# Kernel optimization log

Measured on AMD Instinct MI355X. Metric: run time of the kernel, lower is better.

The kernel has to match this reference:

```python
import jax, jax.numpy as jnp
import numpy as np

B, L, H, E = 32, 256, 8, 16
SEQ_LEN = 64          # init seq_len, used only in final view
OUT = 256             # out_channels, must be divisible by SEQ_LEN
A = E + 1 + 128       # augmented channels: original + time + conv(128)
SIG_CH = A + A * A    # depth-2 signature channels
DN = ('NWC', 'WIO', 'NWC')


def setup_inputs() -> dict:
    key = jax.random.key(0)
    ks = jax.random.split(key, 8)
    return {
        'q': jax.random.normal(ks[0], (B, L, H, E), jnp.float32),
        'k': jax.random.normal(ks[1], (B, L, H, E), jnp.float32),
        'v': jax.random.normal(ks[2], (B, L, H, E), jnp.float32),
        'mask': jnp.zeros((B, L), jnp.bool_),
        'conv1_w': jax.random.normal(ks[3], (3, E, 64), jnp.float32) * 0.1,
        'conv1_b': jnp.zeros((64,), jnp.float32),
        'conv2_w': jax.random.normal(ks[4], (1, 64, 128), jnp.float32) * 0.1,
        'conv2_b': jnp.zeros((128,), jnp.float32),
        'lin_w': jax.random.normal(ks[5], (SIG_CH, OUT), jnp.float32) * 0.01,
        'lin_b': jnp.zeros((OUT,), jnp.float32),
    }


def _signature_depth2(p):
    # p: [N, S, C] piecewise-linear path. Returns [N, C + C*C].
    dx = p[:, 1:] - p[:, :-1]                       # [N, S-1, C]
    s1 = dx.sum(axis=1)                             # level 1
    cum_excl = jnp.cumsum(dx, axis=1) - dx          # sum of increments before t
    # level 2: sum_{s<t} dx_s (x) dx_t + 0.5 * dx_t (x) dx_t
    s2 = jnp.einsum('nti,ntj->nij', cum_excl + 0.5 * dx, dx)
    return jnp.concatenate([s1, s2.reshape(s2.shape[0], -1)], axis=-1)


def reference(q, k, v, mask, conv1_w, conv1_b, conv2_w, conv2_b, lin_w, lin_b):
    Bq, Lq, Hq, Eq = q.shape
    x = q.transpose(0, 2, 1, 3).reshape(Bq * Hq, Lq, Eq)   # [N, L, E]
    T = Lq - 3 + 1                                          # valid-conv length, kernel 3
    # Augment pieces
    trunc = x[:, 2:]                                        # [N, T, E]
    time = jnp.broadcast_to(jnp.linspace(0.0, 1.0, T, dtype=x.dtype)[None, :, None],
                            (Bq * Hq, T, 1))
    a = jax.lax.conv_general_dilated(x, conv1_w, (1,), 'VALID', dimension_numbers=DN) + conv1_b
    a = jax.nn.relu(jax.lax.conv_general_dilated(a, conv2_w, (1,), 'VALID', dimension_numbers=DN) + conv2_b)
    aug = jnp.concatenate([trunc, time, a], axis=2)         # [N, T, A]
    # lead-lag transform as written in source: interleave along time -> [N, 2T, A]
    lag = jnp.concatenate([aug[:, 1:], aug[:, -1:]], axis=1)
    ll = jnp.stack([aug, lag], axis=2).reshape(aug.shape[0], 2 * T, aug.shape[2])
    sig = _signature_depth2(ll)                             # [N, SIG_CH]
    out = sig @ lin_w + lin_b                               # [N, OUT]
    return out.reshape(Bq, Hq, SEQ_LEN, -1)
```

## Files before the change

kernel.cpp:

```cpp
#include <hip/hip_runtime.h>
#include <hip/hip_bf16.h>

#define Bq 32
#define Lq 256
#define Hq 8
#define Eq 16
#define Nn (Bq*Hq)
#define T 254
#define A 145
#define SIG_CH (A + A*A)
#define KP 21184
#define OUT 256

typedef __attribute__((ext_vector_type(8))) short short8;
typedef __attribute__((ext_vector_type(8))) unsigned short ushort8;
typedef __attribute__((ext_vector_type(4))) float floatx4;

static __device__ __forceinline__ unsigned short f2bf(float v) {
    unsigned int u = __float_as_uint(v);
    unsigned int r = (u + 0x7FFFu + ((u >> 16) & 1u)) >> 16;
    return (unsigned short)r;
}
static __device__ __forceinline__ float bf2f(unsigned short b) {
    return __uint_as_float(((unsigned int)b) << 16);
}

__global__ __launch_bounds__(256) void wsplit_kernel(
    const float* __restrict__ w1, const float* __restrict__ w2,
    unsigned short* __restrict__ w1im_hi, unsigned short* __restrict__ w1im_lo,
    unsigned short* __restrict__ w2t_hi,  unsigned short* __restrict__ w2t_lo)
{
    int idx = blockIdx.x*256 + threadIdx.x;
    if (idx < 4096) {
        int c = idx & 63, k = idx >> 6;
        float v = (k < 48) ? w1[k*64 + c] : 0.f;
        unsigned short hb = f2bf(v);
        w1im_hi[c*64 + k] = hb;
        w1im_lo[c*64 + k] = f2bf(v - bf2f(hb));
    } else {
        int j = idx - 4096;
        int c = j & 127, i = j >> 7;
        float v = w2[i*128 + c];
        unsigned short hb = f2bf(v);
        w2t_hi[c*64 + i] = hb;
        w2t_lo[c*64 + i] = f2bf(v - bf2f(hb));
    }
}

#define MDS 40
#define OS3 36
#define XIS 72

__global__ __launch_bounds__(256) void augsig_kernel(
    const float* __restrict__ q,
    const float* __restrict__ b1, const float* __restrict__ b2,
    const unsigned short* __restrict__ w1im_hi, const unsigned short* __restrict__ w1im_lo,
    const unsigned short* __restrict__ w2t_hi,  const unsigned short* __restrict__ w2t_lo,
    unsigned short* __restrict__ sig_hi, unsigned short* __restrict__ sig_lo)
{
    __shared__ __align__(16) unsigned short mdb[3*160*MDS];
    __shared__ __align__(16) float outs[A*OS3];
    __shared__ __align__(16) float xsc[36*16];
    __shared__ __align__(16) float b1s[64];
    __shared__ __align__(16) float b2s[128];

    unsigned short* Mh = mdb;
    unsigned short* Ml = mdb + 160*MDS;
    unsigned short* Dh = mdb + 2*160*MDS;
    unsigned short* ximh = mdb;
    unsigned short* ximl = mdb + 3456;
    unsigned short* a1h  = mdb + 6912;
    unsigned short* a1l  = mdb + 10368;

    const int tid = threadIdx.x;
    const int n = blockIdx.x;
    const int b = n >> 3, h = n & 7;

    const int lane = tid & 63;
    const int wv   = tid >> 6;
    const int frow = lane & 15;
    const int quad = lane >> 4;
    const int wm = wv & 1, wn = wv >> 1;

    if (tid < 64)  b1s[tid] = b1[tid];
    if (tid < 128) b2s[tid] = b2[tid];

    const float4* q4 = (const float4*)q + ((long)(b*Lq)*Hq + h)*4;
    const float inv253 = 1.0f / 253.0f;

    float a0 = 0.f, vlast = 0.f;

    floatx4 acc[5][5];
    #pragma unroll
    for (int i = 0; i < 5; ++i)
        #pragma unroll
        for (int j = 0; j < 5; ++j)
            acc[i][j] = (floatx4){0.f, 0.f, 0.f, 0.f};

    #pragma unroll 1
    for (int c = 0; c < 8; ++c) {
        const int t0 = c*32;

        if (tid < 140) {
            int r = tid >> 2, e4 = tid & 3;
            int t = t0 + r; if (t > 255) t = 255;
            *((float4*)xsc + (r*4 + e4)) = q4[t*32 + e4];
        }
        __syncthreads();

        for (int idx = tid; idx < 48*8; idx += 256) {
            int r = idx >> 3, g = idx & 7;
            unsigned short hh[8], ll[8];
            if (r <= 32 && g < 6) {
                const float* src = &xsc[r*16 + g*8];
                #pragma unroll
                for (int e = 0; e < 8; ++e) {
                    float v = src[e];
                    unsigned short hbv = f2bf(v);
                    hh[e] = hbv; ll[e] = f2bf(v - bf2f(hbv));
                }
            } else {
                #pragma unroll
                for (int e = 0; e < 8; ++e) { hh[e] = 0; ll[e] = 0; }
            }
            *(ushort8*)&ximh[r*XIS + g*8] = *(ushort8*)hh;
            *(ushort8*)&ximl[r*XIS + g*8] = *(ushort8*)ll;
        }
        __syncthreads();

        {
            short8 ah[3][2], al[3][2];
            #pragma unroll
            for (int mt = 0; mt < 3; ++mt)
                #pragma unroll
                for (int ks = 0; ks < 2; ++ks) {
                    int ar = (mt*16 + frow)*XIS + ks*32 + quad*8;
                    ah[mt][ks] = *(const short8*)&ximh[ar];
                    al[mt][ks] = *(const short8*)&ximl[ar];
                }
            short8 bh[2], bl[2];
            #pragma unroll
            for (int ks = 0; ks < 2; ++ks) {
                int br = (wv*16 + frow)*64 + ks*32 + quad*8;
                bh[ks] = *(const short8*)(w1im_hi + br);
                bl[ks] = *(const short8*)(w1im_lo + br);
            }
            floatx4 acc1[3];
            #pragma unroll
            for (int mt = 0; mt < 3; ++mt) acc1[mt] = (floatx4){0.f,0.f,0.f,0.f};
            #pragma unroll
            for (int mt = 0; mt < 3; ++mt)
                #pragma unroll
                for (int ks = 0; ks < 2; ++ks) {
                    acc1[mt] = __builtin_amdgcn_mfma_f32_16x16x32_bf16(ah[mt][ks], bh[ks], acc1[mt], 0,0,0);
                    acc1[mt] = __builtin_amdgcn_mfma_f32_16x16x32_bf16(ah[mt][ks], bl[ks], acc1[mt], 0,0,0);
                    acc1[mt] = __builtin_amdgcn_mfma_f32_16x16x32_bf16(al[mt][ks], bh[ks], acc1[mt], 0,0,0);
                }
            const int cc = wv*16 + frow;
            const float bias = b1s[cc];
            #pragma unroll
            for (int mt = 0; mt < 3; ++mt)
                #pragma unroll
                for (int e = 0; e < 4; ++e) {
                    int t = mt*16 + quad*4 + e;
                    float v = acc1[mt][e] + bias;
                    unsigned short hbv = f2bf(v);
                    a1h[t*XIS + cc] = hbv;
                    a1l[t*XIS + cc] = f2bf(v - bf2f(hbv));
                }
        }
        __syncthreads();

        {
            short8 ah[3][2], al[3][2];
            #pragma unroll
            for (int mt = 0; mt < 3; ++mt)
                #pragma unroll
                for (int ks = 0; ks < 2; ++ks) {
                    int ar = (mt*16 + frow)*XIS + ks*32 + quad*8;
                    ah[mt][ks] = *(const short8*)&a1h[ar];
                    al[mt][ks] = *(const short8*)&a1l[ar];
                }
            short8 bh[2][2], bl[2][2];
            #pragma unroll
            for (int nt = 0; nt < 2; ++nt)
                #pragma unroll
                for (int ks = 0; ks < 2; ++ks) {
                    int br = (wv*32 + nt*16 + frow)*64 + ks*32 + quad*8;
                    bh[nt][ks] = *(const short8*)(w2t_hi + br);
                    bl[nt][ks] = *(const short8*)(w2t_lo + br);
                }
            floatx4 acc2[3][2];
            #pragma unroll
            for (int mt = 0; mt < 3; ++mt)
                #pragma unroll
                for (int nt = 0; nt < 2; ++nt)
                    acc2[mt][nt] = (floatx4){0.f,0.f,0.f,0.f};
            #pragma unroll
            for (int mt = 0; mt < 3; ++mt)
                #pragma unroll
                for (int nt = 0; nt < 2; ++nt)
                    #pragma unroll
                    for (int ks = 0; ks < 2; ++ks) {
                        acc2[mt][nt] = __builtin_amdgcn_mfma_f32_16x16x32_bf16(ah[mt][ks], bh[nt][ks], acc2[mt][nt], 0,0,0);
                        acc2[mt][nt] = __builtin_amdgcn_mfma_f32_16x16x32_bf16(ah[mt][ks], bl[nt][ks], acc2[mt][nt], 0,0,0);
                        acc2[mt][nt] = __builtin_amdgcn_mfma_f32_16x16x32_bf16(al[mt][ks], bh[nt][ks], acc2[mt][nt], 0,0,0);
                    }
            #pragma unroll
            for (int mt = 0; mt < 3; ++mt)
                #pragma unroll
                for (int nt = 0; nt < 2; ++nt) {
                    int cc = wv*32 + nt*16 + frow;
                    float bias = b2s[cc];
                    int tb = mt*16 + quad*4;
                    if (tb <= 32) {
                        float4 vv;
                        vv.x = fmaxf(acc2[mt][nt][0] + bias, 0.f);
                        vv.y = fmaxf(acc2[mt][nt][1] + bias, 0.f);
                        vv.z = fmaxf(acc2[mt][nt][2] + bias, 0.f);
                        vv.w = fmaxf(acc2[mt][nt][3] + bias, 0.f);
                        *(float4*)&outs[(17 + cc)*OS3 + tb] = vv;
                    }
                }
        }
        for (int idx = tid; idx < 17*33; idx += 256) {
            int ch = idx / 33, tt = idx - ch*33;
            float val = (ch < 16) ? xsc[(tt+2)*16 + ch] : (float)(t0+tt)*inv253;
            outs[ch*OS3 + tt] = val;
        }
        __syncthreads();

        if (tid < 160) {
            unsigned short mh[32], ml[32], dh[32];
            if (tid < A) {
                float v[33];
                #pragma unroll
                for (int i = 0; i < 8; ++i)
                    *(float4*)&v[i*4] = *(const float4*)&outs[tid*OS3 + i*4];
                v[32] = outs[tid*OS3 + 32];
                if (c == 0) a0 = v[0];
                if (c == 7) vlast = v[29];
                #pragma unroll
                for (int tl = 0; tl < 32; ++tl) {
                    bool valid = (t0 + tl) <= 252;
                    float x0 = v[tl], x1 = v[tl+1];
                    float d = valid ? (x1 - x0) : 0.f;
                    float m = valid ? (0.5f*(x0 + x1) - a0) : 0.f;
                    unsigned short hbv = f2bf(m);
                    mh[tl] = hbv; ml[tl] = f2bf(m - bf2f(hbv));
                    dh[tl] = f2bf(d);
                }
            } else {
                #pragma unroll
                for (int tl = 0; tl < 32; ++tl) { mh[tl]=0; ml[tl]=0; dh[tl]=0; }
            }
            #pragma unroll
            for (int pp = 0; pp < 4; ++pp) {
                *(ushort8*)&Mh[tid*MDS + pp*8] = *(ushort8*)&mh[pp*8];
                *(ushort8*)&Ml[tid*MDS + pp*8] = *(ushort8*)&ml[pp*8];
                *(ushort8*)&Dh[tid*MDS + pp*8] = *(ushort8*)&dh[pp*8];
            }
        }
        __syncthreads();

        {
            short8 afh[5], afl[5], bfh[5];
            #pragma unroll
            for (int i = 0; i < 5; ++i) {
                int ar = (wm*80 + i*16 + frow)*MDS + quad*8;
                int br = (wn*80 + i*16 + frow)*MDS + quad*8;
                afh[i] = *(const short8*)&Mh[ar];
                afl[i] = *(const short8*)&Ml[ar];
                bfh[i] = *(const short8*)&Dh[br];
            }
            #pragma unroll
            for (int mt = 0; mt < 5; ++mt)
                #pragma unroll
                for (int nt = 0; nt < 5; ++nt) {
                    acc[mt][nt] = __builtin_amdgcn_mfma_f32_16x16x32_bf16(
                        afh[mt], bfh[nt], acc[mt][nt], 0, 0, 0);
                    acc[mt][nt] = __builtin_amdgcn_mfma_f32_16x16x32_bf16(
                        afl[mt], bfh[nt], acc[mt][nt], 0, 0, 0);
                }
        }
    }

    unsigned short* sh = sig_hi + (long)n*KP;
    unsigned short* sl = sig_lo + (long)n*KP;
    if (tid < A) {
        float v = vlast - a0;
        unsigned short hbv = f2bf(v);
        sh[tid] = hbv;
        sl[tid] = f2bf(v - bf2f(hbv));
    }
    if (tid >= 160 && tid < 160 + (KP - SIG_CH)) {
        sh[SIG_CH + tid - 160] = 0;
        sl[SIG_CH + tid - 160] = 0;
    }
    #pragma unroll
    for (int mt = 0; mt < 5; ++mt)
        #pragma unroll
        for (int nt = 0; nt < 5; ++nt) {
            int j = wn*80 + nt*16 + frow;
            int ib = wm*80 + mt*16 + quad*4;
            #pragma unroll
            for (int e = 0; e < 4; ++e) {
                int i = ib + e;
                if (i < A && j < A) {
                    float v = acc[mt][nt][e];
                    unsigned short hbv = f2bf(v);
                    sh[A + i*A + j] = hbv;
                    sl[A + i*A + j] = f2bf(v - bf2f(hbv));
                }
            }
        }
}

__global__ __launch_bounds__(256) void wconv_kernel(
    const float* __restrict__ W,
    unsigned short* __restrict__ wt_hi, unsigned short* __restrict__ wt_lo)
{
    __shared__ float ls[64][65];
    const int tid = threadIdx.x;
    const int k0 = blockIdx.x * 64;
    const int o0 = blockIdx.y * 64;

    #pragma unroll
    for (int p = 0; p < 16; ++p) {
        int idx = tid + p*256;
        int kk = idx >> 6, oo = idx & 63;
        int k = k0 + kk;
        ls[kk][oo] = (k < SIG_CH) ? W[(long)k*OUT + o0 + oo] : 0.f;
    }
    __syncthreads();

    const int ob = tid >> 3;
    const int kq = (tid & 7) * 8;
    #pragma unroll
    for (int p = 0; p < 2; ++p) {
        int o = p*32 + ob;
        unsigned short hbuf[8], lbuf[8];
        #pragma unroll
        for (int j = 0; j < 8; ++j) {
            float v = ls[kq + j][o];
            unsigned short hb = f2bf(v);
            hbuf[j] = hb;
            lbuf[j] = f2bf(v - bf2f(hb));
        }
        long off = (long)(o0 + o)*KP + k0 + kq;
        *(ushort8*)(wt_hi + off) = *(ushort8*)hbuf;
        *(ushort8*)(wt_lo + off) = *(ushort8*)lbuf;
    }
}

#define SPLITK 61
#define KC 352
#define NSTEP (KC/32)
#define LDA 40

__global__ __launch_bounds__(256) void gemm_kernel(
    const unsigned short* __restrict__ sig_hi, const unsigned short* __restrict__ sig_lo,
    const unsigned short* __restrict__ wt_hi,  const unsigned short* __restrict__ wt_lo,
    float* __restrict__ part)
{
    __shared__ __align__(16) unsigned short Ah[128*LDA];
    __shared__ __align__(16) unsigned short Al[128*LDA];
    __shared__ __align__(16) unsigned short Bh[64*LDA];
    __shared__ __align__(16) unsigned short Bl[64*LDA];

    const int tid = threadIdx.x;
    const int o0 = blockIdx.x * 64;
    const int n0 = blockIdx.y * 128;
    const int z  = blockIdx.z;
    const int k0 = z * KC;

    const int lane = tid & 63;
    const int w    = tid >> 6;
    const int wm   = w & 1;
    const int wn   = w >> 1;
    const int frow = lane & 15;
    const int quad = lane >> 4;

    const int srowA = tid >> 1;
    const int khA   = (tid & 1) * 16;
    const int srowB = tid >> 2;
    const int kqB   = (tid & 3) * 8;

    const unsigned short* gAh = sig_hi + (long)(n0 + srowA)*KP;
    const unsigned short* gAl = sig_lo + (long)(n0 + srowA)*KP;
    const unsigned short* gBh = wt_hi  + (long)(o0 + srowB)*KP;
    const unsigned short* gBl = wt_lo  + (long)(o0 + srowB)*KP;

    ushort8 rah[2], ral[2], rbh, rbl;
    const ushort8 z8 = {0,0,0,0,0,0,0,0};

    #define GLOAD(s)                                                          \
        {                                                                     \
            int kb = k0 + (s)*32;                                             \
            if (kb < KP) {                                                    \
                rah[0] = *(const ushort8*)(gAh + kb + khA);                   \
                rah[1] = *(const ushort8*)(gAh + kb + khA + 8);               \
                ral[0] = *(const ushort8*)(gAl + kb + khA);                   \
                ral[1] = *(const ushort8*)(gAl + kb + khA + 8);               \
                rbh    = *(const ushort8*)(gBh + kb + kqB);                   \
                rbl    = *(const ushort8*)(gBl + kb + kqB);                   \
            } else {                                                          \
                rah[0]=z8; rah[1]=z8; ral[0]=z8; ral[1]=z8;                   \
                rbh=z8; rbl=z8;                                               \
            }                                                                 \
        }

    #define LSTORE()                                                          \
        {                                                                     \
            int oA = srowA*LDA + khA;                                         \
            *(ushort8*)(Ah + oA)     = rah[0];                                \
            *(ushort8*)(Ah + oA + 8) = rah[1];                                \
            *(ushort8*)(Al + oA)     = ral[0];                                \
            *(ushort8*)(Al + oA + 8) = ral[1];                                \
            int oB = srowB*LDA + kqB;                                         \
            *(ushort8*)(Bh + oB) = rbh;                                       \
            *(ushort8*)(Bl + oB) = rbl;                                       \
        }

    floatx4 acc[4][2];
    #pragma unroll
    for (int i = 0; i < 4; ++i)
        #pragma unroll
        for (int j = 0; j < 2; ++j)
            acc[i][j] = (floatx4){0.f, 0.f, 0.f, 0.f};

    GLOAD(0);
    LSTORE();
    __syncthreads();

    for (int s = 0; s < NSTEP; ++s) {
        if (s < NSTEP-1) GLOAD(s+1);

        short8 afh[4], afl[4], bfh[2], bfl[2];
        const int aoff = (wm*64 + frow)*LDA + quad*8;
        const int boff = (wn*32 + frow)*LDA + quad*8;
        #pragma unroll
        for (int tI = 0; tI < 4; ++tI) {
            afh[tI] = *(const short8*)(Ah + aoff + tI*16*LDA);
            afl[tI] = *(const short8*)(Al + aoff + tI*16*LDA);
        }
        #pragma unroll
        for (int tI = 0; tI < 2; ++tI) {
            bfh[tI] = *(const short8*)(Bh + boff + tI*16*LDA);
            bfl[tI] = *(const short8*)(Bl + boff + tI*16*LDA);
        }
        #pragma unroll
        for (int mt = 0; mt < 4; ++mt)
            #pragma unroll
            for (int nt = 0; nt < 2; ++nt) {
                acc[mt][nt] = __builtin_amdgcn_mfma_f32_16x16x32_bf16(
                    afh[mt], bfh[nt], acc[mt][nt], 0, 0, 0);
                acc[mt][nt] = __builtin_amdgcn_mfma_f32_16x16x32_bf16(
                    afh[mt], bfl[nt], acc[mt][nt], 0, 0, 0);
                acc[mt][nt] = __builtin_amdgcn_mfma_f32_16x16x32_bf16(
                    afl[mt], bfh[nt], acc[mt][nt], 0, 0, 0);
            }
        __syncthreads();
        if (s < NSTEP-1) {
            LSTORE();
            __syncthreads();
        }
    }

    float* pz = part + (long)z * (Nn*OUT);
    #pragma unroll
    for (int mt = 0; mt < 4; ++mt)
        #pragma unroll
        for (int nt = 0; nt < 2; ++nt) {
            int col = o0 + wn*32 + nt*16 + frow;
            int rbase = n0 + wm*64 + mt*16 + quad*4;
            #pragma unroll
            for (int e = 0; e < 4; ++e)
                pz[(long)(rbase + e)*OUT + col] = acc[mt][nt][e];
        }
}

__global__ __launch_bounds__(256) void reduce_kernel(
    const float* __restrict__ part, const float* __restrict__ lb,
    float* __restrict__ out)
{
    int idx = blockIdx.x * 256 + threadIdx.x;
    float s = lb[idx & 255];
    #pragma unroll 8
    for (int z = 0; z < SPLITK; ++z)
        s += part[(long)z * (Nn*OUT) + idx];
    out[idx] = s;
}

extern "C" void kernel_launch(void* const* d_in, const int* in_sizes, int n_in,
                              void* d_out, int out_size, void* d_ws, size_t ws_size,
                              hipStream_t stream) {
    const float* q  = (const float*)d_in[0];
    const float* w1 = (const float*)d_in[4];
    const float* b1 = (const float*)d_in[5];
    const float* w2 = (const float*)d_in[6];
    const float* b2 = (const float*)d_in[7];
    const float* lw = (const float*)d_in[8];
    const float* lb = (const float*)d_in[9];
    float* out = (float*)d_out;

    char* ws = (char*)d_ws;
    unsigned short* sig_hi  = (unsigned short*)ws;
    unsigned short* sig_lo  = (unsigned short*)(ws + 10846208);
    unsigned short* wt_hi   = (unsigned short*)(ws + 21692416);
    unsigned short* wt_lo   = (unsigned short*)(ws + 32538624);
    float*          part    = (float*)(ws + 43384832);
    unsigned short* w1im_hi = (unsigned short*)(ws + 43384832);
    unsigned short* w1im_lo = (unsigned short*)(ws + 43384832 + 8192);
    unsigned short* w2t_hi  = (unsigned short*)(ws + 43384832 + 16384);
    unsigned short* w2t_lo  = (unsigned short*)(ws + 43384832 + 32768);

    wsplit_kernel<<<48, 256, 0, stream>>>(w1, w2, w1im_hi, w1im_lo, w2t_hi, w2t_lo);
    augsig_kernel<<<Nn, 256, 0, stream>>>(q, b1, b2, w1im_hi, w1im_lo, w2t_hi, w2t_lo, sig_hi, sig_lo);
    wconv_kernel<<<dim3(KP/64, OUT/64), 256, 0, stream>>>(lw, wt_hi, wt_lo);
    gemm_kernel<<<dim3(4, 2, SPLITK), 256, 0, stream>>>(sig_hi, sig_lo, wt_hi, wt_lo, part);
    reduce_kernel<<<(Nn*OUT)/256, 256, 0, stream>>>(part, lb, out);
}
```

Baseline: 170.4 us.

## Merge weight-prep kernels and replace split-K reduce with atomic accumulation

Folds the conv-weight split, the linear-weight bf16 hi/lo conversion, and the bias initialisation of the output into one launch. The split-K GEMM now atomically adds its partials straight into the bias-initialised output, which removes the partial buffer and the separate reduce kernel. This saves two launches and the write and re-read of 61 partial slabs. In exchange there is atomic contention on the output (61 adds per element) and the float summation order becomes nondeterministic.

```diff
diff --git a/kernel.cpp b/kernel.cpp
--- a/kernel.cpp
+++ b/kernel.cpp
@@ -25,25 +25,69 @@
     return __uint_as_float(((unsigned int)b) << 16);
 }
 
-__global__ __launch_bounds__(256) void wsplit_kernel(
+__global__ __launch_bounds__(256) void wprep_kernel(
+    const float* __restrict__ W,
+    unsigned short* __restrict__ wt_hi, unsigned short* __restrict__ wt_lo,
     const float* __restrict__ w1, const float* __restrict__ w2,
     unsigned short* __restrict__ w1im_hi, unsigned short* __restrict__ w1im_lo,
-    unsigned short* __restrict__ w2t_hi,  unsigned short* __restrict__ w2t_lo)
+    unsigned short* __restrict__ w2t_hi,  unsigned short* __restrict__ w2t_lo,
+    const float* __restrict__ lb, float* __restrict__ out)
 {
-    int idx = blockIdx.x*256 + threadIdx.x;
-    if (idx < 4096) {
-        int c = idx & 63, k = idx >> 6;
-        float v = (k < 48) ? w1[k*64 + c] : 0.f;
-        unsigned short hb = f2bf(v);
-        w1im_hi[c*64 + k] = hb;
-        w1im_lo[c*64 + k] = f2bf(v - bf2f(hb));
-    } else {
-        int j = idx - 4096;
-        int c = j & 127, i = j >> 7;
-        float v = w2[i*128 + c];
-        unsigned short hb = f2bf(v);
-        w2t_hi[c*64 + i] = hb;
-        w2t_lo[c*64 + i] = f2bf(v - bf2f(hb));
+    const int tid = threadIdx.x;
+    const int bid = blockIdx.x;
+
+    if (bid >= 1372) {
+        out[(bid - 1372)*256 + tid] = lb[tid];
+        return;
+    }
+    if (bid >= 1324) {
+        int idx = (bid - 1324)*256 + tid;
+        if (idx < 4096) {
+            int c = idx & 63, k = idx >> 6;
+            float v = (k < 48) ? w1[k*64 + c] : 0.f;
+            unsigned short hb = f2bf(v);
+            w1im_hi[c*64 + k] = hb;
+            w1im_lo[c*64 + k] = f2bf(v - bf2f(hb));
+        } else {
+            int j = idx - 4096;
+            int c = j & 127, i = j >> 7;
+            float v = w2[i*128 + c];
+            unsigned short hb = f2bf(v);
+            w2t_hi[c*64 + i] = hb;
+            w2t_lo[c*64 + i] = f2bf(v - bf2f(hb));
+        }
+        return;
+    }
+
+    __shared__ float ls[64][65];
+    const int k0 = (bid % 331) * 64;
+    const int o0 = (bid / 331) * 64;
+
+    #pragma unroll
+    for (int p = 0; p < 16; ++p) {
+        int idx = tid + p*256;
+        int kk = idx >> 6, oo = idx & 63;
+        int k = k0 + kk;
+        ls[kk][oo] = (k < SIG_CH) ? W[(long)k*OUT + o0 + oo] : 0.f;
+    }
+    __syncthreads();
+
+    const int ob = tid >> 3;
+    const int kq = (tid & 7) * 8;
+    #pragma unroll
+    for (int p = 0; p < 2; ++p) {
+        int o = p*32 + ob;
+        unsigned short hbuf[8], lbuf[8];
+        #pragma unroll
+        for (int j = 0; j < 8; ++j) {
+            float v = ls[kq + j][o];
+            unsigned short hb = f2bf(v);
+            hbuf[j] = hb;
+            lbuf[j] = f2bf(v - bf2f(hb));
+        }
+        long off = (long)(o0 + o)*KP + k0 + kq;
+        *(ushort8*)(wt_hi + off) = *(ushort8*)hbuf;
+        *(ushort8*)(wt_lo + off) = *(ushort8*)lbuf;
     }
 }
 
@@ -316,43 +360,6 @@
         }
 }
 
-__global__ __launch_bounds__(256) void wconv_kernel(
-    const float* __restrict__ W,
-    unsigned short* __restrict__ wt_hi, unsigned short* __restrict__ wt_lo)
-{
-    __shared__ float ls[64][65];
-    const int tid = threadIdx.x;
-    const int k0 = blockIdx.x * 64;
-    const int o0 = blockIdx.y * 64;
-
-    #pragma unroll
-    for (int p = 0; p < 16; ++p) {
-        int idx = tid + p*256;
-        int kk = idx >> 6, oo = idx & 63;
-        int k = k0 + kk;
-        ls[kk][oo] = (k < SIG_CH) ? W[(long)k*OUT + o0 + oo] : 0.f;
-    }
-    __syncthreads();
-
-    const int ob = tid >> 3;
-    const int kq = (tid & 7) * 8;
-    #pragma unroll
-    for (int p = 0; p < 2; ++p) {
-        int o = p*32 + ob;
-        unsigned short hbuf[8], lbuf[8];
-        #pragma unroll
-        for (int j = 0; j < 8; ++j) {
-            float v = ls[kq + j][o];
-            unsigned short hb = f2bf(v);
-            hbuf[j] = hb;
-            lbuf[j] = f2bf(v - bf2f(hb));
-        }
-        long off = (long)(o0 + o)*KP + k0 + kq;
-        *(ushort8*)(wt_hi + off) = *(ushort8*)hbuf;
-        *(ushort8*)(wt_lo + off) = *(ushort8*)lbuf;
-    }
-}
-
 #define SPLITK 61
 #define KC 352
 #define NSTEP (KC/32)
@@ -361,7 +368,7 @@
 __global__ __launch_bounds__(256) void gemm_kernel(
     const unsigned short* __restrict__ sig_hi, const unsigned short* __restrict__ sig_lo,
     const unsigned short* __restrict__ wt_hi,  const unsigned short* __restrict__ wt_lo,
-    float* __restrict__ part)
+    float* __restrict__ out)
 {
     __shared__ __align__(16) unsigned short Ah[128*LDA];
     __shared__ __align__(16) unsigned short Al[128*LDA];
@@ -467,7 +474,6 @@
         }
     }
 
-    float* pz = part + (long)z * (Nn*OUT);
     #pragma unroll
     for (int mt = 0; mt < 4; ++mt)
         #pragma unroll
@@ -476,20 +482,8 @@
             int rbase = n0 + wm*64 + mt*16 + quad*4;
             #pragma unroll
             for (int e = 0; e < 4; ++e)
-                pz[(long)(rbase + e)*OUT + col] = acc[mt][nt][e];
-        }
-}
-
-__global__ __launch_bounds__(256) void reduce_kernel(
-    const float* __restrict__ part, const float* __restrict__ lb,
-    float* __restrict__ out)
-{
-    int idx = blockIdx.x * 256 + threadIdx.x;
-    float s = lb[idx & 255];
-    #pragma unroll 8
-    for (int z = 0; z < SPLITK; ++z)
-        s += part[(long)z * (Nn*OUT) + idx];
-    out[idx] = s;
+                atomicAdd(&out[(long)(rbase + e)*OUT + col], acc[mt][nt][e]);
+        }
 }
 
 extern "C" void kernel_launch(void* const* d_in, const int* in_sizes, int n_in,
@@ -509,15 +503,14 @@
     unsigned short* sig_lo  = (unsigned short*)(ws + 10846208);
     unsigned short* wt_hi   = (unsigned short*)(ws + 21692416);
     unsigned short* wt_lo   = (unsigned short*)(ws + 32538624);
-    float*          part    = (float*)(ws + 43384832);
     unsigned short* w1im_hi = (unsigned short*)(ws + 43384832);
     unsigned short* w1im_lo = (unsigned short*)(ws + 43384832 + 8192);
     unsigned short* w2t_hi  = (unsigned short*)(ws + 43384832 + 16384);
     unsigned short* w2t_lo  = (unsigned short*)(ws + 43384832 + 32768);
 
-    wsplit_kernel<<<48, 256, 0, stream>>>(w1, w2, w1im_hi, w1im_lo, w2t_hi, w2t_lo);
+    wprep_kernel<<<1628, 256, 0, stream>>>(lw, wt_hi, wt_lo,
+                                           w1, w2, w1im_hi, w1im_lo, w2t_hi, w2t_lo,
+                                           lb, out);
     augsig_kernel<<<Nn, 256, 0, stream>>>(q, b1, b2, w1im_hi, w1im_lo, w2t_hi, w2t_lo, sig_hi, sig_lo);
-    wconv_kernel<<<dim3(KP/64, OUT/64), 256, 0, stream>>>(lw, wt_hi, wt_lo);
-    gemm_kernel<<<dim3(4, 2, SPLITK), 256, 0, stream>>>(sig_hi, sig_lo, wt_hi, wt_lo, part);
-    reduce_kernel<<<(Nn*OUT)/256, 256, 0, stream>>>(part, lb, out);
+    gemm_kernel<<<dim3(4, 2, SPLITK), 256, 0, stream>>>(sig_hi, sig_lo, wt_hi, wt_lo, out);
 }
```

Result: no change. 168.9 us (-0.9%).
